# Optimization experiments

Hardware: AMD Instinct MI355X
Metric: run time of the kernel (lower is better)

The kernel has to match this reference:

```python
import jax, jax.numpy as jnp
import numpy as np

B, T, F, H = 4096, 48, 64, 128


def _uniform(key, shape, stdv):
    return jax.random.uniform(key, shape, jnp.float32, -stdv, stdv)


def setup_inputs() -> dict:
    key = jax.random.key(0)
    ks = jax.random.split(key, 24)
    values = jax.random.normal(ks[0], (B, T, F), jnp.float32)
    masks = (jax.random.uniform(ks[1], (B, T, F)) < 0.8).astype(jnp.float32)
    deltas = jax.random.uniform(ks[2], (B, T, F), jnp.float32)
    sH = 1.0 / np.sqrt(H)
    sF = 1.0 / np.sqrt(F)
    inp = {
        "values": values, "masks": masks, "deltas": deltas,
        # TemporalDecay h: W [H, F], b [H] (stdv = 1/sqrt(out=H))
        "Wdh": _uniform(ks[3], (H, F), sH), "bdh": _uniform(ks[4], (H,), sH),
        # TemporalDecay x (diag): W [F, F], b [F]
        "Wdx": _uniform(ks[5], (F, F), sF), "bdx": _uniform(ks[6], (F,), sF),
        # hist_reg: Linear(H -> F)
        "Wh": _uniform(ks[7], (F, H), sH), "bh": _uniform(ks[8], (F,), sH),
        # feat_reg: masked F x F
        "Wf": _uniform(ks[9], (F, F), sF), "bf": _uniform(ks[10], (F,), sF),
        # weight_combine: Linear(2F -> F)
        "Wc": _uniform(ks[11], (F, 2 * F), 1.0 / np.sqrt(2 * F)),
        "bc": _uniform(ks[12], (F,), 1.0 / np.sqrt(2 * F)),
        # LSTMCell(2F -> H): gates in PyTorch order i, f, g, o
        "W_ih": _uniform(ks[13], (4 * H, 2 * F), sH),
        "W_hh": _uniform(ks[14], (4 * H, H), sH),
        "b_ih": _uniform(ks[15], (4 * H,), sH),
        "b_hh": _uniform(ks[16], (4 * H,), sH),
        # out: Linear(H -> 1)
        "Wo": _uniform(ks[17], (1, H), sH), "bo": _uniform(ks[18], (1,), sH),
    }
    return inp


def reference(values, masks, deltas, Wdh, bdh, Wdx, bdx, Wh, bh, Wf, bf,
              Wc, bc, W_ih, W_hh, b_ih, b_hh, Wo, bo):
    impute_weight = 1.0
    b, t, f = values.shape
    h_dim = Wdh.shape[0]
    eye = jnp.eye(f, dtype=values.dtype)
    Wdx_m = Wdx * eye            # diagonal temporal decay
    Wf_m = Wf * (1.0 - eye)

    def step(carry, xt):
        h, c, loss = carry
        x, m, d = xt  # each [B, F]
        gamma_h = jnp.exp(-jax.nn.relu(d @ Wdh.T + bdh))        # [B, H]
        gamma_x = jnp.exp(-jax.nn.relu(d @ Wdx_m.T + bdx))      # [B, F]
        h = h * gamma_h
        x_h = h @ Wh.T + bh
        denom = jnp.sum(m) + 1e-5
        loss = loss + jnp.sum(jnp.abs(x - x_h) * m) / denom
        x_c = m * x + (1.0 - m) * x_h
        z_h = x_c @ Wf_m.T + bf
        loss = loss + jnp.sum(jnp.abs(x - z_h) * m) / denom
        alpha = jnp.concatenate([gamma_x, m], axis=1) @ Wc.T + bc
        c_h = alpha * z_h + (1.0 - alpha) * x_h
        loss = loss + jnp.sum(jnp.abs(x - c_h) * m) / denom
        c_c = m * x + (1.0 - m) * c_h
        inputs = jnp.concatenate([c_c, m], axis=1)  # [B, 2F]
        gates = inputs @ W_ih.T + b_ih + h @ W_hh.T + b_hh
        i_g, f_g, g_g, o_g = jnp.split(gates, 4, axis=1)
        c = jax.nn.sigmoid(f_g) * c + jax.nn.sigmoid(i_g) * jnp.tanh(g_g)
        h = jax.nn.sigmoid(o_g) * jnp.tanh(c)
        return (h, c, loss), c_c

    init = (jnp.zeros((b, h_dim), values.dtype),
            jnp.zeros((b, h_dim), values.dtype),
            jnp.zeros((), values.dtype))
    xs = (jnp.swapaxes(values, 0, 1),
          jnp.swapaxes(masks, 0, 1),
          jnp.swapaxes(deltas, 0, 1))
    (h, c, x_loss), imps = jax.lax.scan(step, init, xs)
    imputations = jnp.swapaxes(imps, 0, 1)  # [B, T, F]
    predictions = h @ Wo.T + bo             # [B, 1]
    return x_loss * impute_weight, imputations, predictions
```

## Files before the change

kernel.cpp:

```cpp
#include <hip/hip_runtime.h>
#include <hip/hip_bf16.h>
#include <math.h>

#define BB 4096
#define TT 48
#define FF 64
#define HH 128
#define ROWS 16
#define NT 512
#define NBLK (BB / ROWS)

typedef __attribute__((ext_vector_type(8))) short short8;
typedef __attribute__((ext_vector_type(4))) float f32x4;

__device__ __forceinline__ float sigm(float x) { return 1.f / (1.f + __expf(-x)); }
__device__ __forceinline__ float tanh_f(float x) { return 2.f / (1.f + __expf(-2.f * x)) - 1.f; }

__global__ __launch_bounds__(256) void prep_kernel(
    const float* __restrict__ W_ih, const float* __restrict__ W_hh,
    const float* __restrict__ Wdh,  const float* __restrict__ Wh,
    const float* __restrict__ Wf,   const float* __restrict__ Wc,
    __hip_bfloat16* __restrict__ frags) {
    const int idx = blockIdx.x * 256 + threadIdx.x;
    float v;
    if (idx < 131072) {
        const int jj = idx & 7;
        const int lane = (idx >> 3) & 63;
        const int ks = (idx >> 9) & 7;
        const int tile = idx >> 12;
        const int n = tile * 16 + (lane & 15);
        const int k = ks * 32 + ((lane >> 4) << 3) + jj;
        v = (k < 128) ? W_ih[n * 128 + k] : W_hh[n * 128 + (k - 128)];
    } else {
        const int u = idx - 131072;
        const int jj = u & 7;
        const int lane = (u >> 3) & 63;
        const int lq = lane & 15, q8 = (lane >> 4) << 3;
        if (u < 8192) {
            const int ks = (u >> 9) & 1, nt = u >> 10;
            const int n = nt * 16 + lq, k = ks * 32 + q8 + jj;
            v = Wdh[n * 64 + k];
        } else if (u < 16384) {
            const int uu = u - 8192;
            const int ks = (uu >> 9) & 3, nt = uu >> 11;
            const int n = nt * 16 + lq, k = ks * 32 + q8 + jj;
            v = Wh[n * 128 + k];
        } else if (u < 20480) {
            const int uu = u - 16384;
            const int ks = (uu >> 9) & 1, nt = uu >> 10;
            const int n = nt * 16 + lq, k = ks * 32 + q8 + jj;
            v = (k == n) ? 0.f : Wf[n * 64 + k];
        } else {
            const int uu = u - 20480;
            const int ks = (uu >> 9) & 3, nt = uu >> 11;
            const int n = nt * 16 + lq, k = ks * 32 + q8 + jj;
            v = Wc[n * 128 + k];
        }
    }
    frags[idx] = __float2bfloat16(v);
}

__global__ __launch_bounds__(256) void denom1_kernel(const float* __restrict__ masks,
                                                     float* __restrict__ partials) {
    const int t = blockIdx.x >> 5;
    const int s = blockIdx.x & 31;
    const int tid = threadIdx.x;
    float acc = 0.f;
    #pragma unroll
    for (int k = 0; k < 8; ++k) {
        const int i = k * 256 + tid;
        const int b = s * 128 + (i >> 4);
        const int f = (i & 15) << 2;
        const float4 v = *(const float4*)&masks[((size_t)b * TT + t) * FF + f];
        acc += v.x + v.y + v.z + v.w;
    }
    #pragma unroll
    for (int off = 32; off; off >>= 1) acc += __shfl_down(acc, off, 64);
    __shared__ float red[4];
    if ((tid & 63) == 0) red[tid >> 6] = acc;
    __syncthreads();
    if (tid == 0) partials[blockIdx.x] = red[0] + red[1] + red[2] + red[3];
}

__global__ __launch_bounds__(64) void denom2_kernel(const float* __restrict__ partials,
                                                    float* __restrict__ inv_denom) {
    const int t = threadIdx.x;
    if (t < TT) {
        float s = 0.f;
        #pragma unroll
        for (int i = 0; i < 32; ++i) s += partials[t * 32 + i];
        inv_denom[t] = 1.f / (s + 1e-5f);
    }
}

__global__ __launch_bounds__(NT, 2) void rits_kernel(
    const float* __restrict__ values, const float* __restrict__ masks,
    const float* __restrict__ deltas,
    const float* __restrict__ Wdx, const float* __restrict__ bdx,
    const float* __restrict__ bdh, const float* __restrict__ bh,
    const float* __restrict__ bf,  const float* __restrict__ bc,
    const float* __restrict__ b_ih, const float* __restrict__ b_hh,
    const float* __restrict__ Wo,  const float* __restrict__ bo,
    const __hip_bfloat16* __restrict__ frags,
    const float* __restrict__ inv_denom,
    float* __restrict__ ws_lossblk,
    float* __restrict__ out_imp, float* __restrict__ out_pred)
{
    __shared__ __hip_bfloat16 dbuf[ROWS][72];
    __shared__ __hip_bfloat16 xcbuf[ROWS][72];
    __shared__ __hip_bfloat16 hbufA[ROWS][136];
    __shared__ __hip_bfloat16 hbufB[ROWS][136];
    __shared__ __hip_bfloat16 gxm[ROWS][136];
    __shared__ __hip_bfloat16 ccm[ROWS][136];
    __shared__ float x_lds[ROWS][65];
    __shared__ float m_lds[ROWS][65];
    __shared__ float redl[8];

    const int tid = threadIdx.x;
    const int bid = blockIdx.x;
    const int b0 = bid * ROWS;
    const int lane = tid & 63;
    const int wv = tid >> 6;
    const int quad = lane >> 4;
    const int lq = lane & 15;

    for (int i = tid; i < ROWS * 136; i += NT) ((unsigned short*)hbufA)[i] = 0;

    const float wdx_l = Wdx[lane * (FF + 1)];
    const float bdx_l = bdx[lane];

    const int j_ln = wv * 16 + lq;
    const float bI = b_ih[j_ln]       + b_hh[j_ln];
    const float bF = b_ih[128 + j_ln] + b_hh[128 + j_ln];
    const float bG = b_ih[256 + j_ln] + b_hh[256 + j_ln];
    const float bO = b_ih[384 + j_ln] + b_hh[384 + j_ln];

    const int f46 = (wv & 3) * 16 + lq;
    const float bh_f = bh[f46];
    const float bf_f = bf[f46];
    const float bc_f = bc[f46];

    const float bdh0 = bdh[(wv & 3) * 32 + lq];
    const float bdh1 = bdh[(wv & 3) * 32 + 16 + lq];

    const short8* f8 = (const short8*)frags;

    float c_reg[4];
    #pragma unroll
    for (int r = 0; r < 4; ++r) c_reg[r] = 0.f;
    float loss_acc = 0.f;

    float xn[2], mn[2], dn[2];
    #pragma unroll
    for (int q = 0; q < 2; ++q) {
        const int r = wv + 8 * q;
        const int off = ((b0 + r) * TT + 0) * FF + lane;
        xn[q] = values[off]; mn[q] = masks[off]; dn[q] = deltas[off];
    }
    #pragma unroll
    for (int q = 0; q < 2; ++q) {
        const int r = wv + 8 * q;
        x_lds[r][lane] = xn[q];
        m_lds[r][lane] = mn[q];
        dbuf[r][lane] = __float2bfloat16(dn[q]);
        const float gx = __expf(-fmaxf(fmaf(dn[q], wdx_l, bdx_l), 0.f));
        gxm[r][lane] = __float2bfloat16(gx);
        gxm[r][64 + lane] = __float2bfloat16(mn[q]);
    }
    __syncthreads();

    for (int t = 0; t < TT; ++t) {
        const float invd = inv_denom[t];

        #pragma unroll
        for (int q = 0; q < 2; ++q)
            ccm[wv + 8 * q][64 + lane] = __float2bfloat16(mn[q]);

        float al_r[4];
        if (wv < 4) {
            f32x4 acc = {0.f, 0.f, 0.f, 0.f};
            #pragma unroll
            for (int ks = 0; ks < 4; ++ks) {
                const short8 a = *(const short8*)&gxm[lq][ks * 32 + quad * 8];
                const short8 b = f8[18944 + ((wv * 4 + ks) << 6) + lane];
                acc = __builtin_amdgcn_mfma_f32_16x16x32_bf16(a, b, acc, 0, 0, 0);
            }
            #pragma unroll
            for (int r = 0; r < 4; ++r) al_r[r] = acc[r] + bc_f;
        } else {
            #pragma unroll
            for (int u = 0; u < 2; ++u) {
                const int tile = (wv - 4) * 2 + u;
                f32x4 acc = {0.f, 0.f, 0.f, 0.f};
                #pragma unroll
                for (int ks = 0; ks < 2; ++ks) {
                    const short8 a = *(const short8*)&dbuf[lq][ks * 32 + quad * 8];
                    const short8 b = f8[16384 + ((tile * 2 + ks) << 6) + lane];
                    acc = __builtin_amdgcn_mfma_f32_16x16x32_bf16(a, b, acc, 0, 0, 0);
                }
                const int col = tile * 16 + lq;
                const float bdh_c = (u == 0) ? bdh0 : bdh1;
                #pragma unroll
                for (int r = 0; r < 4; ++r) {
                    const int row = quad * 4 + r;
                    const float gh = __expf(-fmaxf(acc[r] + bdh_c, 0.f));
                    const float hd = __bfloat162float(hbufA[row][col]) * gh;
                    hbufB[row][col] = __float2bfloat16(hd);
                }
            }
        }
        {
            const int tn = (t < TT - 1) ? t + 1 : t;
            #pragma unroll
            for (int q = 0; q < 2; ++q) {
                const int r = wv + 8 * q;
                const int off = ((b0 + r) * TT + tn) * FF + lane;
                xn[q] = values[off]; mn[q] = masks[off]; dn[q] = deltas[off];
            }
        }
        __syncthreads();

        float xv_r[4], mv_r[4], xh_r[4];
        float stepsum = 0.f;
        if (wv < 4) {
            f32x4 acc = {0.f, 0.f, 0.f, 0.f};
            #pragma unroll
            for (int ks = 0; ks < 4; ++ks) {
                const short8 a = *(const short8*)&hbufB[lq][ks * 32 + quad * 8];
                const short8 b = f8[17408 + ((wv * 4 + ks) << 6) + lane];
                acc = __builtin_amdgcn_mfma_f32_16x16x32_bf16(a, b, acc, 0, 0, 0);
            }
            #pragma unroll
            for (int r = 0; r < 4; ++r) {
                const int row = quad * 4 + r;
                const float xh = acc[r] + bh_f;
                xh_r[r] = xh;
                const float xv = x_lds[row][f46], mv = m_lds[row][f46];
                xv_r[r] = xv; mv_r[r] = mv;
                stepsum += mv * fabsf(xv - xh);
                xcbuf[row][f46] = __float2bfloat16(fmaf(mv, xv, (1.f - mv) * xh));
            }
        }
        __syncthreads();

        if (wv < 4) {
            f32x4 acc5 = {0.f, 0.f, 0.f, 0.f};
            #pragma unroll
            for (int ks = 0; ks < 2; ++ks) {
                const short8 a = *(const short8*)&xcbuf[lq][ks * 32 + quad * 8];
                const short8 b = f8[18432 + ((wv * 2 + ks) << 6) + lane];
                acc5 = __builtin_amdgcn_mfma_f32_16x16x32_bf16(a, b, acc5, 0, 0, 0);
            }
            #pragma unroll
            for (int r = 0; r < 4; ++r) {
                const int row = quad * 4 + r;
                const float zh = acc5[r] + bf_f;
                stepsum += mv_r[r] * fabsf(xv_r[r] - zh);
                const float alpha = al_r[r];
                const float ch = fmaf(alpha, zh, (1.f - alpha) * xh_r[r]);
                stepsum += mv_r[r] * fabsf(xv_r[r] - ch);
                const float cc = fmaf(mv_r[r], xv_r[r], (1.f - mv_r[r]) * ch);
                ccm[row][f46] = __float2bfloat16(cc);
                out_imp[((b0 + row) * TT + t) * FF + f46] = cc;
            }
        }
        loss_acc = fmaf(stepsum, invd, loss_acc);
        __syncthreads();

        {
            f32x4 acc[4];
            #pragma unroll
            for (int g = 0; g < 4; ++g) acc[g] = (f32x4){0.f, 0.f, 0.f, 0.f};
            #pragma unroll
            for (int ks = 0; ks < 8; ++ks) {
                const short8 a = (ks < 4)
                    ? *(const short8*)&ccm[lq][ks * 32 + quad * 8]
                    : *(const short8*)&hbufB[lq][(ks - 4) * 32 + quad * 8];
                #pragma unroll
                for (int g = 0; g < 4; ++g) {
                    const short8 b = f8[(((g * 8 + wv) * 8 + ks) << 6) + lane];
                    acc[g] = __builtin_amdgcn_mfma_f32_16x16x32_bf16(a, b, acc[g], 0, 0, 0);
                }
            }
            #pragma unroll
            for (int q = 0; q < 2; ++q) {
                const int r = wv + 8 * q;
                x_lds[r][lane] = xn[q];
                m_lds[r][lane] = mn[q];
                dbuf[r][lane] = __float2bfloat16(dn[q]);
                const float gx = __expf(-fmaxf(fmaf(dn[q], wdx_l, bdx_l), 0.f));
                gxm[r][lane] = __float2bfloat16(gx);
                gxm[r][64 + lane] = __float2bfloat16(mn[q]);
            }
            #pragma unroll
            for (int r = 0; r < 4; ++r) {
                const float ig = sigm(acc[0][r] + bI);
                const float fg = sigm(acc[1][r] + bF);
                const float gg = tanh_f(acc[2][r] + bG);
                const float og = sigm(acc[3][r] + bO);
                c_reg[r] = fmaf(fg, c_reg[r], ig * gg);
                hbufA[quad * 4 + r][j_ln] = __float2bfloat16(og * tanh_f(c_reg[r]));
            }
        }
        __syncthreads();
    }

    {
        const int r = tid >> 5, l = tid & 31;
        float s = 0.f;
        #pragma unroll
        for (int k = l; k < HH; k += 32) s += __bfloat162float(hbufA[r][k]) * Wo[k];
        #pragma unroll
        for (int off = 16; off; off >>= 1) s += __shfl_down(s, off, 32);
        if (l == 0) out_pred[b0 + r] = s + bo[0];
    }
    #pragma unroll
    for (int off = 32; off; off >>= 1) loss_acc += __shfl_down(loss_acc, off, 64);
    if (lane == 0) redl[wv] = loss_acc;
    __syncthreads();
    if (tid == 0) {
        float s = 0.f;
        #pragma unroll
        for (int w = 0; w < 8; ++w) s += redl[w];
        ws_lossblk[bid] = s;
    }
}

__global__ __launch_bounds__(256) void final_kernel(const float* __restrict__ ws_lossblk,
                                                    float* __restrict__ out_loss) {
    const int tid = threadIdx.x;
    float s = ws_lossblk[tid];
    #pragma unroll
    for (int off = 32; off; off >>= 1) s += __shfl_down(s, off, 64);
    __shared__ float red[4];
    if ((tid & 63) == 0) red[tid >> 6] = s;
    __syncthreads();
    if (tid == 0) out_loss[0] = red[0] + red[1] + red[2] + red[3];
}

extern "C" void kernel_launch(void* const* d_in, const int* in_sizes, int n_in,
                              void* d_out, int out_size, void* d_ws, size_t ws_size,
                              hipStream_t stream) {
    const float* values = (const float*)d_in[0];
    const float* masks  = (const float*)d_in[1];
    const float* deltas = (const float*)d_in[2];
    const float* Wdh  = (const float*)d_in[3];
    const float* bdh  = (const float*)d_in[4];
    const float* Wdx  = (const float*)d_in[5];
    const float* bdx  = (const float*)d_in[6];
    const float* Wh   = (const float*)d_in[7];
    const float* bh   = (const float*)d_in[8];
    const float* Wf   = (const float*)d_in[9];
    const float* bf   = (const float*)d_in[10];
    const float* Wc   = (const float*)d_in[11];
    const float* bc   = (const float*)d_in[12];
    const float* W_ih = (const float*)d_in[13];
    const float* W_hh = (const float*)d_in[14];
    const float* b_ih = (const float*)d_in[15];
    const float* b_hh = (const float*)d_in[16];
    const float* Wo   = (const float*)d_in[17];
    const float* bo   = (const float*)d_in[18];

    __hip_bfloat16* frags = (__hip_bfloat16*)d_ws;
    float* inv_denom  = (float*)((char*)d_ws + 320 * 1024);
    float* partials   = inv_denom + 64;
    float* ws_lossblk = partials + 2048;

    float* out_loss = (float*)d_out;
    float* out_imp  = out_loss + 1;
    float* out_pred = out_imp + (size_t)BB * TT * FF;

    prep_kernel<<<624, 256, 0, stream>>>(W_ih, W_hh, Wdh, Wh, Wf, Wc, frags);
    denom1_kernel<<<TT * 32, 256, 0, stream>>>(masks, partials);
    denom2_kernel<<<1, 64, 0, stream>>>(partials, inv_denom);
    rits_kernel<<<NBLK, NT, 0, stream>>>(
        values, masks, deltas, Wdx, bdx, bdh, bh, bf, bc,
        b_ih, b_hh, Wo, bo, frags, inv_denom, ws_lossblk, out_imp, out_pred);
    final_kernel<<<1, 256, 0, stream>>>(ws_lossblk, out_loss);
}
```

Baseline: 357.3 us.

## Split LSTM gate GEMM across phases and keep h and small weights in registers

The LSTM gate matmul is broken into three K-chunks (h, mask, c_c) that are issued as soon as each input is ready, so MFMA work overlaps the serial imputation chain instead of all running at the end. The hidden state now stays in registers, and every wave computes the gamma_h decay for its own H columns, which removes the hbufA round trip through LDS. The small weight fragments for gamma, alpha, x_h and z_h are preloaded into registers once instead of being reloaded from global memory every step. This raises register pressure at a launch bound of 2 blocks per CU and adds more MFMA work to each phase before the barriers.

```diff
diff --git a/kernel.cpp b/kernel.cpp
--- a/kernel.cpp
+++ b/kernel.cpp
@@ -12,6 +12,8 @@
 
 typedef __attribute__((ext_vector_type(8))) short short8;
 typedef __attribute__((ext_vector_type(4))) float f32x4;
+
+#define MFMA(a, b, c) __builtin_amdgcn_mfma_f32_16x16x32_bf16((a), (b), (c), 0, 0, 0)
 
 __device__ __forceinline__ float sigm(float x) { return 1.f / (1.f + __expf(-x)); }
 __device__ __forceinline__ float tanh_f(float x) { return 2.f / (1.f + __expf(-2.f * x)) - 1.f; }
@@ -107,11 +109,11 @@
     float* __restrict__ out_imp, float* __restrict__ out_pred)
 {
     __shared__ __hip_bfloat16 dbuf[ROWS][72];
+    __shared__ __hip_bfloat16 gxbuf[ROWS][72];
+    __shared__ __hip_bfloat16 mbuf[ROWS][72];
     __shared__ __hip_bfloat16 xcbuf[ROWS][72];
-    __shared__ __hip_bfloat16 hbufA[ROWS][136];
+    __shared__ __hip_bfloat16 ccbuf[ROWS][72];
     __shared__ __hip_bfloat16 hbufB[ROWS][136];
-    __shared__ __hip_bfloat16 gxm[ROWS][136];
-    __shared__ __hip_bfloat16 ccm[ROWS][136];
     __shared__ float x_lds[ROWS][65];
     __shared__ float m_lds[ROWS][65];
     __shared__ float redl[8];
@@ -123,103 +125,111 @@
     const int wv = tid >> 6;
     const int quad = lane >> 4;
     const int lq = lane & 15;
-
-    for (int i = tid; i < ROWS * 136; i += NT) ((unsigned short*)hbufA)[i] = 0;
+    const int wv3 = wv & 3;
 
     const float wdx_l = Wdx[lane * (FF + 1)];
     const float bdx_l = bdx[lane];
 
     const int j_ln = wv * 16 + lq;
+    const float bdh_w = bdh[j_ln];
     const float bI = b_ih[j_ln]       + b_hh[j_ln];
     const float bF = b_ih[128 + j_ln] + b_hh[128 + j_ln];
     const float bG = b_ih[256 + j_ln] + b_hh[256 + j_ln];
     const float bO = b_ih[384 + j_ln] + b_hh[384 + j_ln];
 
-    const int f46 = (wv & 3) * 16 + lq;
+    const int f46 = wv3 * 16 + lq;
     const float bh_f = bh[f46];
     const float bf_f = bf[f46];
     const float bc_f = bc[f46];
 
-    const float bdh0 = bdh[(wv & 3) * 32 + lq];
-    const float bdh1 = bdh[(wv & 3) * 32 + 16 + lq];
-
     const short8* f8 = (const short8*)frags;
 
-    float c_reg[4];
-    #pragma unroll
-    for (int r = 0; r < 4; ++r) c_reg[r] = 0.f;
+    short8 Bgam[2], Bal[4], Bxh[4], Bzh[2];
+    #pragma unroll
+    for (int ks = 0; ks < 2; ++ks) Bgam[ks] = f8[16384 + ((wv * 2 + ks) << 6) + lane];
+    #pragma unroll
+    for (int ks = 0; ks < 4; ++ks) Bal[ks] = f8[18944 + ((wv3 * 4 + ks) << 6) + lane];
+    #pragma unroll
+    for (int ks = 0; ks < 4; ++ks) Bxh[ks] = f8[17408 + ((wv3 * 4 + ks) << 6) + lane];
+    #pragma unroll
+    for (int ks = 0; ks < 2; ++ks) Bzh[ks] = f8[18432 + ((wv3 * 2 + ks) << 6) + lane];
+
+    const int gbase = (wv << 9) + lane;
+
+    float c_reg[4], h_reg[4];
+    #pragma unroll
+    for (int r = 0; r < 4; ++r) { c_reg[r] = 0.f; h_reg[r] = 0.f; }
     float loss_acc = 0.f;
 
-    float xn[2], mn[2], dn[2];
-    #pragma unroll
-    for (int q = 0; q < 2; ++q) {
-        const int r = wv + 8 * q;
-        const int off = ((b0 + r) * TT + 0) * FF + lane;
-        xn[q] = values[off]; mn[q] = masks[off]; dn[q] = deltas[off];
-    }
-    #pragma unroll
-    for (int q = 0; q < 2; ++q) {
-        const int r = wv + 8 * q;
-        x_lds[r][lane] = xn[q];
-        m_lds[r][lane] = mn[q];
-        dbuf[r][lane] = __float2bfloat16(dn[q]);
-        const float gx = __expf(-fmaxf(fmaf(dn[q], wdx_l, bdx_l), 0.f));
-        gxm[r][lane] = __float2bfloat16(gx);
-        gxm[r][64 + lane] = __float2bfloat16(mn[q]);
+    const int base0 = ((b0 + wv) * TT) * FF + lane;
+    const int base1 = ((b0 + wv + 8) * TT) * FF + lane;
+    const int imp0  = ((b0 + quad * 4) * TT) * FF + f46;
+
+    float xn0 = values[base0], mn0 = masks[base0], dn0 = deltas[base0];
+    float xn1 = values[base1], mn1 = masks[base1], dn1 = deltas[base1];
+    {
+        const int r0 = wv, r1 = wv + 8;
+        x_lds[r0][lane] = xn0; m_lds[r0][lane] = mn0;
+        dbuf[r0][lane]  = __float2bfloat16(dn0);
+        gxbuf[r0][lane] = __float2bfloat16(__expf(-fmaxf(fmaf(dn0, wdx_l, bdx_l), 0.f)));
+        mbuf[r0][lane]  = __float2bfloat16(mn0);
+        x_lds[r1][lane] = xn1; m_lds[r1][lane] = mn1;
+        dbuf[r1][lane]  = __float2bfloat16(dn1);
+        gxbuf[r1][lane] = __float2bfloat16(__expf(-fmaxf(fmaf(dn1, wdx_l, bdx_l), 0.f)));
+        mbuf[r1][lane]  = __float2bfloat16(mn1);
     }
     __syncthreads();
 
     for (int t = 0; t < TT; ++t) {
         const float invd = inv_denom[t];
 
-        #pragma unroll
-        for (int q = 0; q < 2; ++q)
-            ccm[wv + 8 * q][64 + lane] = __float2bfloat16(mn[q]);
-
+        {
+            const int tn = (t < TT - 1) ? t + 1 : t;
+            const int o0 = base0 + tn * FF, o1 = base1 + tn * FF;
+            xn0 = values[o0]; mn0 = masks[o0]; dn0 = deltas[o0];
+            xn1 = values[o1]; mn1 = masks[o1]; dn1 = deltas[o1];
+        }
         float al_r[4];
-        if (wv < 4) {
-            f32x4 acc = {0.f, 0.f, 0.f, 0.f};
-            #pragma unroll
-            for (int ks = 0; ks < 4; ++ks) {
-                const short8 a = *(const short8*)&gxm[lq][ks * 32 + quad * 8];
-                const short8 b = f8[18944 + ((wv * 4 + ks) << 6) + lane];
-                acc = __builtin_amdgcn_mfma_f32_16x16x32_bf16(a, b, acc, 0, 0, 0);
-            }
-            #pragma unroll
-            for (int r = 0; r < 4; ++r) al_r[r] = acc[r] + bc_f;
-        } else {
-            #pragma unroll
-            for (int u = 0; u < 2; ++u) {
-                const int tile = (wv - 4) * 2 + u;
-                f32x4 acc = {0.f, 0.f, 0.f, 0.f};
+        {
+            f32x4 ga = {0.f, 0.f, 0.f, 0.f};
+            #pragma unroll
+            for (int ks = 0; ks < 2; ++ks) {
+                const short8 a = *(const short8*)&dbuf[lq][ks * 32 + quad * 8];
+                ga = MFMA(a, Bgam[ks], ga);
+            }
+            if (wv < 4) {
+                f32x4 aa = {0.f, 0.f, 0.f, 0.f};
                 #pragma unroll
                 for (int ks = 0; ks < 2; ++ks) {
-                    const short8 a = *(const short8*)&dbuf[lq][ks * 32 + quad * 8];
-                    const short8 b = f8[16384 + ((tile * 2 + ks) << 6) + lane];
-                    acc = __builtin_amdgcn_mfma_f32_16x16x32_bf16(a, b, acc, 0, 0, 0);
+                    const short8 a = *(const short8*)&gxbuf[lq][ks * 32 + quad * 8];
+                    aa = MFMA(a, Bal[ks], aa);
                 }
-                const int col = tile * 16 + lq;
-                const float bdh_c = (u == 0) ? bdh0 : bdh1;
                 #pragma unroll
-                for (int r = 0; r < 4; ++r) {
-                    const int row = quad * 4 + r;
-                    const float gh = __expf(-fmaxf(acc[r] + bdh_c, 0.f));
-                    const float hd = __bfloat162float(hbufA[row][col]) * gh;
-                    hbufB[row][col] = __float2bfloat16(hd);
+                for (int ks = 2; ks < 4; ++ks) {
+                    const short8 a = *(const short8*)&mbuf[lq][(ks - 2) * 32 + quad * 8];
+                    aa = MFMA(a, Bal[ks], aa);
                 }
-            }
-        }
-        {
-            const int tn = (t < TT - 1) ? t + 1 : t;
-            #pragma unroll
-            for (int q = 0; q < 2; ++q) {
-                const int r = wv + 8 * q;
-                const int off = ((b0 + r) * TT + tn) * FF + lane;
-                xn[q] = values[off]; mn[q] = masks[off]; dn[q] = deltas[off];
+                #pragma unroll
+                for (int r = 0; r < 4; ++r) al_r[r] = aa[r] + bc_f;
+            }
+            #pragma unroll
+            for (int r = 0; r < 4; ++r) {
+                const float gh = __expf(-fmaxf(ga[r] + bdh_w, 0.f));
+                hbufB[quad * 4 + r][j_ln] = __float2bfloat16(h_reg[r] * gh);
             }
         }
         __syncthreads();
 
+        f32x4 gacc0 = {0.f,0.f,0.f,0.f}, gacc1 = {0.f,0.f,0.f,0.f};
+        f32x4 gacc2 = {0.f,0.f,0.f,0.f}, gacc3 = {0.f,0.f,0.f,0.f};
+        #pragma unroll
+        for (int ks = 4; ks < 8; ++ks) {
+            const short8 a = *(const short8*)&hbufB[lq][(ks - 4) * 32 + quad * 8];
+            gacc0 = MFMA(a, f8[gbase + 0     + (ks << 6)], gacc0);
+            gacc1 = MFMA(a, f8[gbase + 4096  + (ks << 6)], gacc1);
+            gacc2 = MFMA(a, f8[gbase + 8192  + (ks << 6)], gacc2);
+            gacc3 = MFMA(a, f8[gbase + 12288 + (ks << 6)], gacc3);
+        }
         float xv_r[4], mv_r[4], xh_r[4];
         float stepsum = 0.f;
         if (wv < 4) {
@@ -227,8 +237,7 @@
             #pragma unroll
             for (int ks = 0; ks < 4; ++ks) {
                 const short8 a = *(const short8*)&hbufB[lq][ks * 32 + quad * 8];
-                const short8 b = f8[17408 + ((wv * 4 + ks) << 6) + lane];
-                acc = __builtin_amdgcn_mfma_f32_16x16x32_bf16(a, b, acc, 0, 0, 0);
+                acc = MFMA(a, Bxh[ks], acc);
             }
             #pragma unroll
             for (int r = 0; r < 4; ++r) {
@@ -243,13 +252,20 @@
         }
         __syncthreads();
 
+        #pragma unroll
+        for (int ks = 2; ks < 4; ++ks) {
+            const short8 a = *(const short8*)&mbuf[lq][(ks - 2) * 32 + quad * 8];
+            gacc0 = MFMA(a, f8[gbase + 0     + (ks << 6)], gacc0);
+            gacc1 = MFMA(a, f8[gbase + 4096  + (ks << 6)], gacc1);
+            gacc2 = MFMA(a, f8[gbase + 8192  + (ks << 6)], gacc2);
+            gacc3 = MFMA(a, f8[gbase + 12288 + (ks << 6)], gacc3);
+        }
         if (wv < 4) {
             f32x4 acc5 = {0.f, 0.f, 0.f, 0.f};
             #pragma unroll
             for (int ks = 0; ks < 2; ++ks) {
                 const short8 a = *(const short8*)&xcbuf[lq][ks * 32 + quad * 8];
-                const short8 b = f8[18432 + ((wv * 2 + ks) << 6) + lane];
-                acc5 = __builtin_amdgcn_mfma_f32_16x16x32_bf16(a, b, acc5, 0, 0, 0);
+                acc5 = MFMA(a, Bzh[ks], acc5);
             }
             #pragma unroll
             for (int r = 0; r < 4; ++r) {
@@ -260,56 +276,53 @@
                 const float ch = fmaf(alpha, zh, (1.f - alpha) * xh_r[r]);
                 stepsum += mv_r[r] * fabsf(xv_r[r] - ch);
                 const float cc = fmaf(mv_r[r], xv_r[r], (1.f - mv_r[r]) * ch);
-                ccm[row][f46] = __float2bfloat16(cc);
-                out_imp[((b0 + row) * TT + t) * FF + f46] = cc;
+                ccbuf[row][f46] = __float2bfloat16(cc);
+                out_imp[imp0 + r * (TT * FF) + t * FF] = cc;
             }
         }
         loss_acc = fmaf(stepsum, invd, loss_acc);
         __syncthreads();
 
+        #pragma unroll
+        for (int ks = 0; ks < 2; ++ks) {
+            const short8 a = *(const short8*)&ccbuf[lq][ks * 32 + quad * 8];
+            gacc0 = MFMA(a, f8[gbase + 0     + (ks << 6)], gacc0);
+            gacc1 = MFMA(a, f8[gbase + 4096  + (ks << 6)], gacc1);
+            gacc2 = MFMA(a, f8[gbase + 8192  + (ks << 6)], gacc2);
+            gacc3 = MFMA(a, f8[gbase + 12288 + (ks << 6)], gacc3);
+        }
         {
-            f32x4 acc[4];
-            #pragma unroll
-            for (int g = 0; g < 4; ++g) acc[g] = (f32x4){0.f, 0.f, 0.f, 0.f};
-            #pragma unroll
-            for (int ks = 0; ks < 8; ++ks) {
-                const short8 a = (ks < 4)
-                    ? *(const short8*)&ccm[lq][ks * 32 + quad * 8]
-                    : *(const short8*)&hbufB[lq][(ks - 4) * 32 + quad * 8];
-                #pragma unroll
-                for (int g = 0; g < 4; ++g) {
-                    const short8 b = f8[(((g * 8 + wv) * 8 + ks) << 6) + lane];
-                    acc[g] = __builtin_amdgcn_mfma_f32_16x16x32_bf16(a, b, acc[g], 0, 0, 0);
-                }
-            }
-            #pragma unroll
-            for (int q = 0; q < 2; ++q) {
-                const int r = wv + 8 * q;
-                x_lds[r][lane] = xn[q];
-                m_lds[r][lane] = mn[q];
-                dbuf[r][lane] = __float2bfloat16(dn[q]);
-                const float gx = __expf(-fmaxf(fmaf(dn[q], wdx_l, bdx_l), 0.f));
-                gxm[r][lane] = __float2bfloat16(gx);
-                gxm[r][64 + lane] = __float2bfloat16(mn[q]);
-            }
-            #pragma unroll
-            for (int r = 0; r < 4; ++r) {
-                const float ig = sigm(acc[0][r] + bI);
-                const float fg = sigm(acc[1][r] + bF);
-                const float gg = tanh_f(acc[2][r] + bG);
-                const float og = sigm(acc[3][r] + bO);
-                c_reg[r] = fmaf(fg, c_reg[r], ig * gg);
-                hbufA[quad * 4 + r][j_ln] = __float2bfloat16(og * tanh_f(c_reg[r]));
-            }
+            const int r0 = wv, r1 = wv + 8;
+            x_lds[r0][lane] = xn0; m_lds[r0][lane] = mn0;
+            dbuf[r0][lane]  = __float2bfloat16(dn0);
+            gxbuf[r0][lane] = __float2bfloat16(__expf(-fmaxf(fmaf(dn0, wdx_l, bdx_l), 0.f)));
+            mbuf[r0][lane]  = __float2bfloat16(mn0);
+            x_lds[r1][lane] = xn1; m_lds[r1][lane] = mn1;
+            dbuf[r1][lane]  = __float2bfloat16(dn1);
+            gxbuf[r1][lane] = __float2bfloat16(__expf(-fmaxf(fmaf(dn1, wdx_l, bdx_l), 0.f)));
+            mbuf[r1][lane]  = __float2bfloat16(mn1);
+        }
+        #pragma unroll
+        for (int r = 0; r < 4; ++r) {
+            const float ig = sigm(gacc0[r] + bI);
+            const float fg = sigm(gacc1[r] + bF);
+            const float gg = tanh_f(gacc2[r] + bG);
+            const float og = sigm(gacc3[r] + bO);
+            c_reg[r] = fmaf(fg, c_reg[r], ig * gg);
+            h_reg[r] = og * tanh_f(c_reg[r]);
         }
         __syncthreads();
     }
 
+    #pragma unroll
+    for (int r = 0; r < 4; ++r)
+        hbufB[quad * 4 + r][j_ln] = __float2bfloat16(h_reg[r]);
+    __syncthreads();
     {
         const int r = tid >> 5, l = tid & 31;
         float s = 0.f;
         #pragma unroll
-        for (int k = l; k < HH; k += 32) s += __bfloat162float(hbufA[r][k]) * Wo[k];
+        for (int k = l; k < HH; k += 32) s += __bfloat162float(hbufB[r][k]) * Wo[k];
         #pragma unroll
         for (int off = 16; off; off >>= 1) s += __shfl_down(s, off, 32);
         if (l == 0) out_pred[b0 + r] = s + bo[0];
```

Result: no change. 362.8 us (+1.5%).
